# Optimization experiments

Measured on AMD Instinct MI355X. Metric: run time of the kernel, lower is better.

The kernel has to match this reference:

```python
import jax, jax.numpy as jnp
import numpy as np

B, S, D, H = 2, 2048, 1024, 16
DK = D // H  # 64


def _quantum(x, W1, b1, W2, b2):
    # Stand-in for QuantumNeuralLayer: classical->quantum->classical, d_k -> d_k.
    return jnp.tanh(x @ W1 + b1) @ W2 + b2


def setup_inputs() -> dict:
    key = jax.random.key(0)
    ks = jax.random.split(key, 16)
    s = 1.0 / np.sqrt(DK)
    inp = {
        "q": jax.random.normal(ks[0], (B, S, D), dtype=jnp.float32),
        "k": jax.random.normal(ks[1], (B, S, D), dtype=jnp.float32),
        "v": jax.random.normal(ks[2], (B, S, D), dtype=jnp.float32),
    }
    names = ["q", "k", "v"]
    for i, n in enumerate(names):
        inp[f"W{n}1"] = jax.random.normal(ks[3 + 4 * i], (DK, DK), dtype=jnp.float32) * s
        inp[f"b{n}1"] = jnp.zeros((DK,), dtype=jnp.float32)
        inp[f"W{n}2"] = jax.random.normal(ks[4 + 4 * i], (DK, DK), dtype=jnp.float32) * s
        inp[f"b{n}2"] = jnp.zeros((DK,), dtype=jnp.float32)
    inp["Wo"] = jax.random.normal(ks[15], (D, D), dtype=jnp.float32) * (1.0 / np.sqrt(D))
    inp["bo"] = jnp.zeros((D,), dtype=jnp.float32)
    return inp


def reference(q, k, v, Wq1, bq1, Wq2, bq2, Wk1, bk1, Wk2, bk2,
              Wv1, bv1, Wv2, bv2, Wo, bo):
    b, s, _ = q.shape
    # split heads: [B, S, H, DK]
    qh = q.reshape(b, s, H, DK)
    kh = k.reshape(b, s, H, DK)
    vh = v.reshape(b, s, H, DK)
    # quantum per-feature transform on last dim
    qh = _quantum(qh, Wq1, bq1, Wq2, bq2)
    kh = _quantum(kh, Wk1, bk1, Wk2, bk2)
    vh = _quantum(vh, Wv1, bv1, Wv2, bv2)
    scale = 1.0 / jnp.sqrt(jnp.asarray(DK, dtype=qh.dtype))
    # scores: [B, H, S, S]
    scores = jnp.einsum("bqhd,bkhd->bhqk", qh, kh) * scale
    attn = jax.nn.softmax(scores, axis=-1)
    # context: [B, H, S, DK] -> [B, S, D]
    ctx = jnp.einsum("bhqk,bkhd->bqhd", attn, vh).reshape(b, s, D)
    return ctx @ Wo + bo
```

## Files before the change

kernel.cpp:

```cpp
#include <hip/hip_runtime.h>

#define B_ 2
#define S_ 2048
#define D_ 1024
#define H_ 16
#define DK_ 64

typedef float f32x4 __attribute__((ext_vector_type(4)));
typedef float f32x16 __attribute__((ext_vector_type(16)));
typedef short bf16x8 __attribute__((ext_vector_type(8)));

static __device__ __forceinline__ unsigned short f2bf(float f) {
  unsigned u = __float_as_uint(f);
  unsigned r = (u + 0x7FFFu + ((u >> 16) & 1u)) >> 16;
  return (unsigned short)r;
}

static __device__ __forceinline__ unsigned cvtpk_bf16(float lo, float hi) {
  unsigned r;
  asm("v_cvt_pk_bf16_f32 %0, %1, %2" : "=v"(r) : "v"(lo), "v"(hi));
  return r;
}

static __device__ __forceinline__ void load16_lds(const void* g, void* lds) {
  __builtin_amdgcn_global_load_lds(
      (const __attribute__((address_space(1))) unsigned int*)g,
      (__attribute__((address_space(3))) unsigned int*)lds, 16, 0, 0);
}

static __device__ __forceinline__ bf16x8 make_pa8(const float* p, int hi) {
  unsigned x1 = cvtpk_bf16(p[0], p[1]);
  unsigned x2 = cvtpk_bf16(p[2], p[3]);
  unsigned y1 = cvtpk_bf16(p[4], p[5]);
  unsigned y2 = cvtpk_bf16(p[6], p[7]);
  unsigned sx1 = (unsigned)__shfl_xor((int)x1, 32);
  unsigned sx2 = (unsigned)__shfl_xor((int)x2, 32);
  unsigned sy1 = (unsigned)__shfl_xor((int)y1, 32);
  unsigned sy2 = (unsigned)__shfl_xor((int)y2, 32);
  union {
    unsigned u[4];
    bf16x8 v;
  } pa;
  pa.u[0] = hi ? sy1 : x1;
  pa.u[1] = hi ? sy2 : x2;
  pa.u[2] = hi ? y1 : sx1;
  pa.u[3] = hi ? y2 : sx2;
  return pa.v;
}

static __device__ __forceinline__ float tanh_fast(float x) {
  float xc = fminf(fmaxf(x, -9.0f), 9.0f);
  float e = exp2f(xc * 2.88539008177792681472f);
  return (e - 1.0f) / (e + 1.0f);
}

__global__ __launch_bounds__(256) void quantum_fused(
    const float* __restrict__ xq, const float* __restrict__ xk,
    const float* __restrict__ xv,
    const float* __restrict__ Wq1, const float* __restrict__ bq1,
    const float* __restrict__ Wq2, const float* __restrict__ bq2,
    const float* __restrict__ Wk1, const float* __restrict__ bk1,
    const float* __restrict__ Wk2, const float* __restrict__ bk2,
    const float* __restrict__ Wv1, const float* __restrict__ bv1,
    const float* __restrict__ Wv2, const float* __restrict__ bv2,
    unsigned short* __restrict__ qhb, unsigned short* __restrict__ khb,
    unsigned short* __restrict__ vtb, float qscale) {
  const int tid = threadIdx.x;
  const int w = tid >> 6;
  const int l = tid & 63;
  const int lq = l & 31;
  const int hi = l >> 5;
  const int bh = blockIdx.y;
  const int b = bh >> 4, h = bh & 15;
  const int s0w = blockIdx.x * 128 + w * 32;

  const float* x;
  const float* W1;
  const float* b1;
  const float* W2;
  const float* b2;
  unsigned short* outp;
  float scale = 1.0f;
  int vmode = 0;
  if (blockIdx.z == 0) {
    x = xq; W1 = Wq1; b1 = bq1; W2 = Wq2; b2 = bq2; outp = qhb;
    scale = qscale;
  } else if (blockIdx.z == 1) {
    x = xk; W1 = Wk1; b1 = bk1; W2 = Wk2; b2 = bk2; outp = khb;
  } else {
    x = xv; W1 = Wv1; b1 = bv1; W2 = Wv2; b2 = bv2; outp = vtb;
    vmode = 1;
  }

  bf16x8 w1f[2][4];
#pragma unroll
  for (int ca = 0; ca < 2; ++ca)
#pragma unroll
    for (int kc = 0; kc < 4; ++kc) {
      const float* wp = W1 + (size_t)(kc * 16 + hi * 8) * 64 + ca * 32 + lq;
      union {
        unsigned u[4];
        bf16x8 v;
      } ww;
#pragma unroll
      for (int jj = 0; jj < 4; ++jj)
        ww.u[jj] = cvtpk_bf16(wp[(2 * jj) * 64], wp[(2 * jj + 1) * 64]);
      w1f[ca][kc] = ww.v;
    }

  const float* xrow = x + (((size_t)b * S_ + s0w + lq) * H_ + h) * DK_;
  bf16x8 xf[4];
#pragma unroll
  for (int kc = 0; kc < 4; ++kc) {
    float4 f0 = *(const float4*)(xrow + kc * 16 + hi * 8);
    float4 f1 = *(const float4*)(xrow + kc * 16 + hi * 8 + 4);
    union {
      unsigned u[4];
      bf16x8 v;
    } xx;
    xx.u[0] = cvtpk_bf16(f0.x, f0.y);
    xx.u[1] = cvtpk_bf16(f0.z, f0.w);
    xx.u[2] = cvtpk_bf16(f1.x, f1.y);
    xx.u[3] = cvtpk_bf16(f1.z, f1.w);
    xf[kc] = xx.v;
  }

  f32x16 acc1[2];
#pragma unroll
  for (int ca = 0; ca < 2; ++ca)
#pragma unroll
    for (int r = 0; r < 16; ++r)
      acc1[ca][r] = b1[ca * 32 + (r & 3) + 8 * (r >> 2) + 4 * hi];
#pragma unroll
  for (int kc = 0; kc < 4; ++kc) {
    acc1[0] = __builtin_amdgcn_mfma_f32_32x32x16_bf16(w1f[0][kc], xf[kc], acc1[0], 0, 0, 0);
    acc1[1] = __builtin_amdgcn_mfma_f32_32x32x16_bf16(w1f[1][kc], xf[kc], acc1[1], 0, 0, 0);
  }

  float t0[16], t1[16];
#pragma unroll
  for (int r = 0; r < 16; ++r) {
    t0[r] = tanh_fast(acc1[0][r]);
    t1[r] = tanh_fast(acc1[1][r]);
  }

  bf16x8 af[4];
  af[0] = make_pa8(&t0[0], hi);
  af[1] = make_pa8(&t0[8], hi);
  af[2] = make_pa8(&t1[0], hi);
  af[3] = make_pa8(&t1[8], hi);

  bf16x8 w2f[2][4];
#pragma unroll
  for (int nb = 0; nb < 2; ++nb)
#pragma unroll
    for (int kc = 0; kc < 4; ++kc) {
      const float* wp = W2 + (size_t)(kc * 16 + hi * 8) * 64 + nb * 32 + lq;
      union {
        unsigned u[4];
        bf16x8 v;
      } ww;
#pragma unroll
      for (int jj = 0; jj < 4; ++jj)
        ww.u[jj] = cvtpk_bf16(wp[(2 * jj) * 64], wp[(2 * jj + 1) * 64]);
      w2f[nb][kc] = ww.v;
    }

  f32x16 acc2[2];
#pragma unroll
  for (int nb = 0; nb < 2; ++nb)
#pragma unroll
    for (int r = 0; r < 16; ++r)
      acc2[nb][r] = b2[nb * 32 + (r & 3) + 8 * (r >> 2) + 4 * hi];
#pragma unroll
  for (int kc = 0; kc < 4; ++kc) {
    acc2[0] = __builtin_amdgcn_mfma_f32_32x32x16_bf16(af[kc], w2f[0][kc], acc2[0], 0, 0, 0);
    acc2[1] = __builtin_amdgcn_mfma_f32_32x32x16_bf16(af[kc], w2f[1][kc], acc2[1], 0, 0, 0);
  }

  if (!vmode) {
#pragma unroll
    for (int nb = 0; nb < 2; ++nb)
#pragma unroll
      for (int r = 0; r < 16; ++r) {
        const int s = s0w + (r & 3) + 8 * (r >> 2) + 4 * hi;
        outp[((size_t)bh * S_ + s) * DK_ + nb * 32 + lq] =
            f2bf(acc2[nb][r] * scale);
      }
  } else {
#pragma unroll
    for (int nb = 0; nb < 2; ++nb) {
      float yv[16];
#pragma unroll
      for (int r = 0; r < 16; ++r) yv[r] = acc2[nb][r];
      const size_t rowb = ((size_t)bh * DK_ + nb * 32 + lq) * S_;
      *(bf16x8*)(outp + rowb + s0w + hi * 8) = make_pa8(&yv[0], hi);
      *(bf16x8*)(outp + rowb + s0w + 16 + hi * 8) = make_pa8(&yv[8], hi);
    }
  }
}

__global__ __launch_bounds__(256, 4) void attn_kernel(
    const unsigned short* __restrict__ qhb,
    const unsigned short* __restrict__ khb,
    const unsigned short* __restrict__ vtb,
    unsigned short* __restrict__ ctxb) {
  __shared__ __align__(16) unsigned short ks_u[2][64 * 64];
  __shared__ __align__(16) unsigned short vs_u[2][64 * 64];

  const int tid = threadIdx.x;
  const int w = tid >> 6;
  const int l = tid & 63;
  const int lq = l & 31;
  const int hi = l >> 5;
  const int khalf = w >> 1;
  const int bh = blockIdx.x;
  const int b = bh >> 4, h = bh & 15;
  const int q0 = blockIdx.y * 64 + (w & 1) * 32;

  const unsigned short* qp = qhb + ((size_t)bh * S_ + q0 + lq) * DK_ + hi * 8;
  bf16x8 qf[4];
#pragma unroll
  for (int kc = 0; kc < 4; ++kc) qf[kc] = *(const bf16x8*)(qp + kc * 16);

  f32x16 o0 = {}, o1 = {};
  f32x16 lacc = {};

  union {
    unsigned u[4];
    bf16x8 v;
  } onesu;
  onesu.u[0] = 0x3F803F80u;
  onesu.u[1] = 0x3F803F80u;
  onesu.u[2] = 0x3F803F80u;
  onesu.u[3] = 0x3F803F80u;
  const bf16x8 ones = onesu.v;

  const unsigned short* kgbase = khb + (size_t)bh * S_ * DK_;
  const unsigned short* vgbase = vtb + (size_t)bh * DK_ * S_;
  const int r0 = w * 16 + (l >> 3);
  const int sl8 = ((l & 7) ^ (l >> 3)) * 8;

  const unsigned short* kp0 = kgbase + (size_t)r0 * DK_ + sl8;
  const unsigned short* kp1 = kp0 + 8 * DK_;
  const unsigned short* vp0 = vgbase + (size_t)r0 * S_ + sl8;
  const unsigned short* vp1 = vp0 + 8 * S_;

#define STAGE(BUF)                                                            \
  {                                                                           \
    char* kb = (char*)ks_u[BUF] + w * 2048;                                   \
    char* vb = (char*)vs_u[BUF] + w * 2048;                                   \
    load16_lds(kp0, kb);                                                      \
    load16_lds(kp1, kb + 1024);                                               \
    load16_lds(vp0, vb);                                                      \
    load16_lds(vp1, vb + 1024);                                               \
    kp0 += 64 * DK_; kp1 += 64 * DK_; vp0 += 64; vp1 += 64;                   \
  }

  STAGE(0)
  __syncthreads();

  const int kr = khalf * 32 + lq;

  for (int t = 0; t < 32; ++t) {
    const int cur = t & 1;
    const char* ksP = (const char*)ks_u[cur];
    const char* vsP = (const char*)vs_u[cur];
    if (t < 31) STAGE(cur ^ 1)

    f32x16 s0;
#pragma unroll
    for (int i = 0; i < 16; ++i) s0[i] = -32.0f;
    __builtin_amdgcn_s_setprio(1);
#pragma unroll
    for (int kc = 0; kc < 4; ++kc) {
      bf16x8 k0 = *(const bf16x8*)(ksP + kr * 128 + (((kc * 2 + hi) ^ (kr & 7)) << 4));
      s0 = __builtin_amdgcn_mfma_f32_32x32x16_bf16(k0, qf[kc], s0, 0, 0, 0);
    }
    __builtin_amdgcn_s_setprio(0);

#pragma unroll
    for (int i = 0; i < 16; ++i) s0[i] = exp2f(s0[i]);

    float pv[8];
    __builtin_amdgcn_s_setprio(1);
#pragma unroll
    for (int kc = 0; kc < 2; ++kc) {
#pragma unroll
      for (int j = 0; j < 8; ++j) pv[j] = s0[kc * 8 + j];
      bf16x8 pav = make_pa8(pv, hi);
      const int slot = khalf * 4 + kc * 2 + hi;
      bf16x8 v0 = *(const bf16x8*)(vsP + lq * 128 + ((slot ^ (lq & 7)) << 4));
      bf16x8 v1 = *(const bf16x8*)(vsP + (32 + lq) * 128 + ((slot ^ (lq & 7)) << 4));
      o0 = __builtin_amdgcn_mfma_f32_32x32x16_bf16(pav, v0, o0, 0, 0, 0);
      o1 = __builtin_amdgcn_mfma_f32_32x32x16_bf16(pav, v1, o1, 0, 0, 0);
      lacc = __builtin_amdgcn_mfma_f32_32x32x16_bf16(pav, ones, lacc, 0, 0, 0);
    }
    __builtin_amdgcn_s_setprio(0);

    __syncthreads();
  }
#undef STAGE

  float* ksf = (float*)&ks_u[0][0];
  float* mlf = (float*)&vs_u[0][0];
  const int qlb = (w & 1) * 32;

  if (khalf == 1) {
#pragma unroll
    for (int r = 0; r < 16; ++r) {
      const int ql = qlb + (r & 3) + 8 * (r >> 2) + 4 * hi;
      ksf[ql * 64 + lq] = o0[r];
      ksf[ql * 64 + 32 + lq] = o1[r];
      if (lq == 0) mlf[ql] = lacc[r];
    }
  }
  __syncthreads();

  if (khalf == 0) {
#pragma unroll
    for (int r = 0; r < 16; ++r) {
      const int crow = ((r & 3) + 8 * (r >> 2)) + 4 * hi;
      const int ql = qlb + crow;
      const float li = 1.0f / (lacc[r] + mlf[ql]);
      const int qg = blockIdx.y * 64 + ql;
      const size_t base = ((size_t)b * S_ + qg) * D_ + h * DK_;
      ctxb[base + lq] = f2bf((o0[r] + ksf[ql * 64 + lq]) * li);
      ctxb[base + 32 + lq] = f2bf((o1[r] + ksf[ql * 64 + 32 + lq]) * li);
    }
  }
}

__global__ __launch_bounds__(256) void wo_transpose(
    const float* __restrict__ Wo, unsigned short* __restrict__ WoT) {
  __shared__ float t[64][65];
  const int k0 = blockIdx.x * 64, n0 = blockIdx.y * 64;
  const int r = threadIdx.x >> 4, c4 = threadIdx.x & 15;
#pragma unroll
  for (int i = 0; i < 4; ++i) {
    float4 v = *(const float4*)&Wo[(size_t)(k0 + r + 16 * i) * D_ + n0 + c4 * 4];
    t[r + 16 * i][c4 * 4 + 0] = v.x;
    t[r + 16 * i][c4 * 4 + 1] = v.y;
    t[r + 16 * i][c4 * 4 + 2] = v.z;
    t[r + 16 * i][c4 * 4 + 3] = v.w;
  }
  __syncthreads();
  const int n = threadIdx.x >> 2, kc = threadIdx.x & 3;
  union {
    unsigned short u[16];
    uint4 v[2];
  } pk;
#pragma unroll
  for (int j = 0; j < 16; ++j) pk.u[j] = f2bf(t[kc * 16 + j][n]);
  unsigned short* op = WoT + (size_t)(n0 + n) * D_ + k0 + kc * 16;
  *(uint4*)op = pk.v[0];
  *(uint4*)(op + 8) = pk.v[1];
}

__global__ __launch_bounds__(256) void out_gemm_mfma(
    const unsigned short* __restrict__ A,
    const unsigned short* __restrict__ BT,
    const float* __restrict__ bo, float* __restrict__ C) {
  __shared__ __align__(16) unsigned short As[3][128 * 64];
  __shared__ __align__(16) unsigned short Bs[3][128 * 64];

  const int tid = threadIdx.x;
  const int w = tid >> 6, l = tid & 63;
  const int ll = l & 15, lg = l >> 4;
  const int wr = w >> 1, wc = w & 1;
  const int m0 = blockIdx.y * 128, n0 = blockIdx.x * 128;

  const int srow = l >> 3;
  const int sslot = (l & 7) ^ srow;
  const int g_off = sslot * 8;

  f32x4 acc[4][4];
#pragma unroll
  for (int mt = 0; mt < 4; ++mt)
#pragma unroll
    for (int nt = 0; nt < 4; ++nt) acc[mt][nt] = (f32x4){0.f, 0.f, 0.f, 0.f};

#define STAGE_G(BUF, KT)                                                      \
  {                                                                           \
    const int k0e = (KT)*64;                                                  \
    _Pragma("unroll") for (int c = 0; c < 4; ++c) {                           \
      const int row = c * 32 + w * 8 + srow;                                  \
      load16_lds(A + (size_t)(m0 + row) * D_ + k0e + g_off,                   \
                 (char*)As[BUF] + c * 4096 + w * 1024);                       \
      load16_lds(BT + (size_t)(n0 + row) * D_ + k0e + g_off,                  \
                 (char*)Bs[BUF] + c * 4096 + w * 1024);                       \
    }                                                                         \
  }

  STAGE_G(0, 0)
  STAGE_G(1, 1)

  for (int kt = 0; kt < 16; ++kt) {
    if (kt < 15) {
      asm volatile("s_waitcnt vmcnt(8)" ::: "memory");
    } else {
      asm volatile("s_waitcnt vmcnt(0)" ::: "memory");
    }
    __builtin_amdgcn_sched_barrier(0);
    __builtin_amdgcn_s_barrier();
    __builtin_amdgcn_sched_barrier(0);

    const int cur = kt % 3;
    if (kt < 14) STAGE_G((kt + 2) % 3, kt + 2)

#pragma unroll
    for (int half = 0; half < 2; ++half) {
      bf16x8 af[4], bfr[4];
#pragma unroll
      for (int mt = 0; mt < 4; ++mt) {
        const int row = wr * 64 + mt * 16 + ll;
        af[mt] = *(const bf16x8*)((const char*)As[cur] + row * 128 +
                                  (((half * 4 + lg) ^ (row & 7)) << 4));
      }
#pragma unroll
      for (int nt = 0; nt < 4; ++nt) {
        const int rowb = wc * 64 + nt * 16 + ll;
        bfr[nt] = *(const bf16x8*)((const char*)Bs[cur] + rowb * 128 +
                                   (((half * 4 + lg) ^ (rowb & 7)) << 4));
      }
      __builtin_amdgcn_s_setprio(1);
#pragma unroll
      for (int mt = 0; mt < 4; ++mt)
#pragma unroll
        for (int nt = 0; nt < 4; ++nt)
          acc[mt][nt] = __builtin_amdgcn_mfma_f32_16x16x32_bf16(
              af[mt], bfr[nt], acc[mt][nt], 0, 0, 0);
      __builtin_amdgcn_s_setprio(0);
    }
  }
#undef STAGE_G

#pragma unroll
  for (int nt = 0; nt < 4; ++nt) {
    const int col = n0 + wc * 64 + nt * 16 + ll;
    const float bv = bo[col];
#pragma unroll
    for (int mt = 0; mt < 4; ++mt) {
      const int row0 = m0 + wr * 64 + mt * 16 + lg * 4;
#pragma unroll
      for (int r = 0; r < 4; ++r)
        C[(size_t)(row0 + r) * D_ + col] = acc[mt][nt][r] + bv;
    }
  }
}

extern "C" void kernel_launch(void* const* d_in, const int* in_sizes, int n_in,
                              void* d_out, int out_size, void* d_ws,
                              size_t ws_size, hipStream_t stream) {
  const float* q = (const float*)d_in[0];
  const float* k = (const float*)d_in[1];
  const float* v = (const float*)d_in[2];
  const float* Wq1 = (const float*)d_in[3];
  const float* bq1 = (const float*)d_in[4];
  const float* Wq2 = (const float*)d_in[5];
  const float* bq2 = (const float*)d_in[6];
  const float* Wk1 = (const float*)d_in[7];
  const float* bk1 = (const float*)d_in[8];
  const float* Wk2 = (const float*)d_in[9];
  const float* bk2 = (const float*)d_in[10];
  const float* Wv1 = (const float*)d_in[11];
  const float* bv1 = (const float*)d_in[12];
  const float* Wv2 = (const float*)d_in[13];
  const float* bv2 = (const float*)d_in[14];
  const float* Wo = (const float*)d_in[15];
  const float* bo = (const float*)d_in[16];
  float* out = (float*)d_out;

  const size_t TEN = (size_t)B_ * H_ * S_ * DK_;
  char* ws = (char*)d_ws;
  unsigned short* qhb = (unsigned short*)ws;
  unsigned short* khb = (unsigned short*)(ws + TEN * 2);
  unsigned short* vtb = (unsigned short*)(ws + TEN * 4);
  unsigned short* ctxb = (unsigned short*)(ws + TEN * 6);
  unsigned short* wot = (unsigned short*)(ws + TEN * 8);

  const float cs = 0.125f * 1.44269504088896340736f;
  quantum_fused<<<dim3(16, 32, 3), 256, 0, stream>>>(
      q, k, v, Wq1, bq1, Wq2, bq2, Wk1, bk1, Wk2, bk2, Wv1, bv1, Wv2, bv2,
      qhb, khb, vtb, cs);
  wo_transpose<<<dim3(16, 16), 256, 0, stream>>>(Wo, wot);

  attn_kernel<<<dim3(32, 32), 256, 0, stream>>>(qhb, khb, vtb, ctxb);

  out_gemm_mfma<<<dim3(8, 32), 256, 0, stream>>>(ctxb, wot, bo, out);
}
```

Before: 115.1 us.

## Double attention query tile per block, fuse Wo transpose, use permlane32 swap

The attention kernel moves to 512-thread blocks covering 128 queries, so each staged K/V tile in LDS is shared by twice as many query rows and global/LDS staging traffic per query drops. The Wo transpose becomes an extra z-slice of the quantum kernel, removing one launch. The bf16 P fragment assembly uses v_permlane32_swap instead of four cross-lane shuffles plus selects. The fixed exponent offset of -32 is dropped, which changes numerics and could risk overflow for large scores; the larger blocks may also reduce occupancy.

```diff
diff --git a/kernel.cpp b/kernel.cpp
--- a/kernel.cpp
+++ b/kernel.cpp
@@ -33,18 +33,17 @@
   unsigned x2 = cvtpk_bf16(p[2], p[3]);
   unsigned y1 = cvtpk_bf16(p[4], p[5]);
   unsigned y2 = cvtpk_bf16(p[6], p[7]);
-  unsigned sx1 = (unsigned)__shfl_xor((int)x1, 32);
-  unsigned sx2 = (unsigned)__shfl_xor((int)x2, 32);
-  unsigned sy1 = (unsigned)__shfl_xor((int)y1, 32);
-  unsigned sy2 = (unsigned)__shfl_xor((int)y2, 32);
+  asm("v_permlane32_swap_b32 %0, %1" : "+v"(x1), "+v"(y1));
+  asm("v_permlane32_swap_b32 %0, %1" : "+v"(x2), "+v"(y2));
   union {
     unsigned u[4];
     bf16x8 v;
   } pa;
-  pa.u[0] = hi ? sy1 : x1;
-  pa.u[1] = hi ? sy2 : x2;
-  pa.u[2] = hi ? y1 : sx1;
-  pa.u[3] = hi ? y2 : sx2;
+  pa.u[0] = x1;
+  pa.u[1] = x2;
+  pa.u[2] = y1;
+  pa.u[3] = y2;
+  (void)hi;
   return pa.v;
 }
 
@@ -63,9 +62,39 @@
     const float* __restrict__ Wk2, const float* __restrict__ bk2,
     const float* __restrict__ Wv1, const float* __restrict__ bv1,
     const float* __restrict__ Wv2, const float* __restrict__ bv2,
+    const float* __restrict__ Wo, unsigned short* __restrict__ WoT,
     unsigned short* __restrict__ qhb, unsigned short* __restrict__ khb,
     unsigned short* __restrict__ vtb, float qscale) {
+  __shared__ float tt[64][65];
+
   const int tid = threadIdx.x;
+
+  if (blockIdx.z == 3) {
+    if (blockIdx.y >= 16) return;
+    const int k0 = blockIdx.x * 64, n0 = blockIdx.y * 64;
+    const int r = tid >> 4, c4 = tid & 15;
+#pragma unroll
+    for (int i = 0; i < 4; ++i) {
+      float4 v = *(const float4*)&Wo[(size_t)(k0 + r + 16 * i) * D_ + n0 + c4 * 4];
+      tt[r + 16 * i][c4 * 4 + 0] = v.x;
+      tt[r + 16 * i][c4 * 4 + 1] = v.y;
+      tt[r + 16 * i][c4 * 4 + 2] = v.z;
+      tt[r + 16 * i][c4 * 4 + 3] = v.w;
+    }
+    __syncthreads();
+    const int n = tid >> 2, kc = tid & 3;
+    union {
+      unsigned short u[16];
+      uint4 v[2];
+    } pk;
+#pragma unroll
+    for (int j = 0; j < 16; ++j) pk.u[j] = f2bf(tt[kc * 16 + j][n]);
+    unsigned short* op = WoT + (size_t)(n0 + n) * D_ + k0 + kc * 16;
+    *(uint4*)op = pk.v[0];
+    *(uint4*)(op + 8) = pk.v[1];
+    return;
+  }
+
   const int w = tid >> 6;
   const int l = tid & 63;
   const int lq = l & 31;
@@ -200,23 +229,24 @@
   }
 }
 
-__global__ __launch_bounds__(256, 4) void attn_kernel(
+__global__ __launch_bounds__(512, 4) void attn_kernel(
     const unsigned short* __restrict__ qhb,
     const unsigned short* __restrict__ khb,
     const unsigned short* __restrict__ vtb,
     unsigned short* __restrict__ ctxb) {
-  __shared__ __align__(16) unsigned short ks_u[2][64 * 64];
-  __shared__ __align__(16) unsigned short vs_u[2][64 * 64];
+  __shared__ __align__(16) unsigned short kvbuf[2][2][64 * 64];
+  __shared__ float mlseg[128];
 
   const int tid = threadIdx.x;
   const int w = tid >> 6;
   const int l = tid & 63;
   const int lq = l & 31;
   const int hi = l >> 5;
-  const int khalf = w >> 1;
+  const int qg = w & 3;
+  const int khalf = w >> 2;
   const int bh = blockIdx.x;
   const int b = bh >> 4, h = bh & 15;
-  const int q0 = blockIdx.y * 64 + (w & 1) * 32;
+  const int q0 = blockIdx.y * 128 + qg * 32;
 
   const unsigned short* qp = qhb + ((size_t)bh * S_ + q0 + lq) * DK_ + hi * 8;
   bf16x8 qf[4];
@@ -238,23 +268,18 @@
 
   const unsigned short* kgbase = khb + (size_t)bh * S_ * DK_;
   const unsigned short* vgbase = vtb + (size_t)bh * DK_ * S_;
-  const int r0 = w * 16 + (l >> 3);
+  const int r0 = w * 8 + (l >> 3);
   const int sl8 = ((l & 7) ^ (l >> 3)) * 8;
 
-  const unsigned short* kp0 = kgbase + (size_t)r0 * DK_ + sl8;
-  const unsigned short* kp1 = kp0 + 8 * DK_;
-  const unsigned short* vp0 = vgbase + (size_t)r0 * S_ + sl8;
-  const unsigned short* vp1 = vp0 + 8 * S_;
+  const unsigned short* kp = kgbase + (size_t)r0 * DK_ + sl8;
+  const unsigned short* vp = vgbase + (size_t)r0 * S_ + sl8;
 
 #define STAGE(BUF)                                                            \
   {                                                                           \
-    char* kb = (char*)ks_u[BUF] + w * 2048;                                   \
-    char* vb = (char*)vs_u[BUF] + w * 2048;                                   \
-    load16_lds(kp0, kb);                                                      \
-    load16_lds(kp1, kb + 1024);                                               \
-    load16_lds(vp0, vb);                                                      \
-    load16_lds(vp1, vb + 1024);                                               \
-    kp0 += 64 * DK_; kp1 += 64 * DK_; vp0 += 64; vp1 += 64;                   \
+    load16_lds(kp, (char*)kvbuf[BUF][0] + w * 1024);                          \
+    load16_lds(vp, (char*)kvbuf[BUF][1] + w * 1024);                          \
+    kp += 64 * DK_;                                                           \
+    vp += 64;                                                                 \
   }
 
   STAGE(0)
@@ -264,13 +289,11 @@
 
   for (int t = 0; t < 32; ++t) {
     const int cur = t & 1;
-    const char* ksP = (const char*)ks_u[cur];
-    const char* vsP = (const char*)vs_u[cur];
+    const char* ksP = (const char*)kvbuf[cur][0];
+    const char* vsP = (const char*)kvbuf[cur][1];
     if (t < 31) STAGE(cur ^ 1)
 
-    f32x16 s0;
-#pragma unroll
-    for (int i = 0; i < 16; ++i) s0[i] = -32.0f;
+    f32x16 s0 = {};
     __builtin_amdgcn_s_setprio(1);
 #pragma unroll
     for (int kc = 0; kc < 4; ++kc) {
@@ -302,9 +325,8 @@
   }
 #undef STAGE
 
-  float* ksf = (float*)&ks_u[0][0];
-  float* mlf = (float*)&vs_u[0][0];
-  const int qlb = (w & 1) * 32;
+  float* ksf = (float*)&kvbuf[0][0][0];
+  const int qlb = qg * 32;
 
   if (khalf == 1) {
 #pragma unroll
@@ -312,7 +334,7 @@
       const int ql = qlb + (r & 3) + 8 * (r >> 2) + 4 * hi;
       ksf[ql * 64 + lq] = o0[r];
       ksf[ql * 64 + 32 + lq] = o1[r];
-      if (lq == 0) mlf[ql] = lacc[r];
+      if (lq == 0) mlseg[ql] = lacc[r];
     }
   }
   __syncthreads();
@@ -322,39 +344,13 @@
     for (int r = 0; r < 16; ++r) {
       const int crow = ((r & 3) + 8 * (r >> 2)) + 4 * hi;
       const int ql = qlb + crow;
-      const float li = 1.0f / (lacc[r] + mlf[ql]);
-      const int qg = blockIdx.y * 64 + ql;
-      const size_t base = ((size_t)b * S_ + qg) * D_ + h * DK_;
+      const float li = 1.0f / (lacc[r] + mlseg[ql]);
+      const int qg_ = blockIdx.y * 128 + ql;
+      const size_t base = ((size_t)b * S_ + qg_) * D_ + h * DK_;
       ctxb[base + lq] = f2bf((o0[r] + ksf[ql * 64 + lq]) * li);
       ctxb[base + 32 + lq] = f2bf((o1[r] + ksf[ql * 64 + 32 + lq]) * li);
     }
   }
-}
-
-__global__ __launch_bounds__(256) void wo_transpose(
-    const float* __restrict__ Wo, unsigned short* __restrict__ WoT) {
-  __shared__ float t[64][65];
-  const int k0 = blockIdx.x * 64, n0 = blockIdx.y * 64;
-  const int r = threadIdx.x >> 4, c4 = threadIdx.x & 15;
-#pragma unroll
-  for (int i = 0; i < 4; ++i) {
-    float4 v = *(const float4*)&Wo[(size_t)(k0 + r + 16 * i) * D_ + n0 + c4 * 4];
-    t[r + 16 * i][c4 * 4 + 0] = v.x;
-    t[r + 16 * i][c4 * 4 + 1] = v.y;
-    t[r + 16 * i][c4 * 4 + 2] = v.z;
-    t[r + 16 * i][c4 * 4 + 3] = v.w;
-  }
-  __syncthreads();
-  const int n = threadIdx.x >> 2, kc = threadIdx.x & 3;
-  union {
-    unsigned short u[16];
-    uint4 v[2];
-  } pk;
-#pragma unroll
-  for (int j = 0; j < 16; ++j) pk.u[j] = f2bf(t[kc * 16 + j][n]);
-  unsigned short* op = WoT + (size_t)(n0 + n) * D_ + k0 + kc * 16;
-  *(uint4*)op = pk.v[0];
-  *(uint4*)(op + 8) = pk.v[1];
 }
 
 __global__ __launch_bounds__(256) void out_gemm_mfma(
@@ -480,12 +476,11 @@
   unsigned short* wot = (unsigned short*)(ws + TEN * 8);
 
   const float cs = 0.125f * 1.44269504088896340736f;
-  quantum_fused<<<dim3(16, 32, 3), 256, 0, stream>>>(
+  quantum_fused<<<dim3(16, 32, 4), 256, 0, stream>>>(
       q, k, v, Wq1, bq1, Wq2, bq2, Wk1, bk1, Wk2, bk2, Wv1, bv1, Wv2, bv2,
-      qhb, khb, vtb, cs);
-  wo_transpose<<<dim3(16, 16), 256, 0, stream>>>(Wo, wot);
-
-  attn_kernel<<<dim3(32, 32), 256, 0, stream>>>(qhb, khb, vtb, ctxb);
+      Wo, wot, qhb, khb, vtb, cs);
+
+  attn_kernel<<<dim3(32, 16), 512, 0, stream>>>(qhb, khb, vtb, ctxb);
 
   out_gemm_mfma<<<dim3(8, 32), 256, 0, stream>>>(ctxb, wot, bo, out);
 }
```

Result: faster. 102.3 us (-11.1%).
